# Kernel optimization log

Hardware: AMD Instinct MI355X
Metric: run time of the kernel (lower is better)

## Reference

```python
import jax, jax.numpy as jnp
import numpy as np

N = 20000      # nodes
E = 640000     # edges
IN = 2         # in_dim
H = 4          # heads
C = 64         # hidden_dim (per-head channels)
ED = 3         # edge_dim
K = 4          # num_clusters
EPS = 1e-16    # PyG softmax eps


def setup_inputs():
    key = jax.random.key(0)
    ks = jax.random.split(key, 32)
    g = lambda i, sh: (jax.random.normal(ks[i], sh, dtype=jnp.float32) * 0.1)
    inp = {
        'x': jax.random.normal(ks[0], (N, IN), dtype=jnp.float32),
        'edge_index': jax.random.randint(ks[1], (2, E), 0, N, dtype=jnp.int64),
        'edge_attr': jax.random.normal(ks[2], (E, ED), dtype=jnp.float32),
        # input_proj
        'Wp': g(3, (IN, C)), 'bp': g(4, (C,)),
        # conv1: in C -> H*C, concat
        'W1': g(5, (C, H * C)), 'We1': g(6, (ED, H * C)),
        'as1': g(7, (H, C)), 'ad1': g(8, (H, C)), 'ae1': g(9, (H, C)), 'b1': g(10, (H * C,)),
        # conv2: in H*C -> H*C, concat
        'W2': g(11, (H * C, H * C)), 'We2': g(12, (ED, H * C)),
        'as2': g(13, (H, C)), 'ad2': g(14, (H, C)), 'ae2': g(15, (H, C)), 'b2': g(16, (H * C,)),
        # conv3: in H*C -> C, heads=1
        'W3': g(17, (H * C, C)), 'We3': g(18, (ED, C)),
        'as3': g(19, (1, C)), 'ad3': g(20, (1, C)), 'ae3': g(21, (1, C)), 'b3': g(22, (C,)),
        # classifier
        'Wc': g(23, (C, K)), 'bc': g(24, (K,)),
    }
    return inp


def _gat(h, src, dst, edge_attr, W, We, a_src, a_dst, a_edge, bias, heads, cph):
    """PyG GATConv (shared lin for src/dst, edge_dim, concat=True), eval mode."""
    xh = (h @ W).reshape(N, heads, cph)                       # [N,H,C]
    alpha_src = jnp.einsum('nhc,hc->nh', xh, a_src)           # [N,H]
    alpha_dst = jnp.einsum('nhc,hc->nh', xh, a_dst)
    eh = (edge_attr @ We).reshape(E, heads, cph)              # [E,H,C]
    alpha = alpha_src[src] + alpha_dst[dst] + jnp.einsum('ehc,hc->eh', eh, a_edge)
    alpha = jax.nn.leaky_relu(alpha, 0.2)                     # [E,H]
    # segment softmax over destination neighborhoods
    m = jax.ops.segment_max(alpha, dst, num_segments=N)       # [N,H]
    ea = jnp.exp(alpha - m[dst])
    s = jax.ops.segment_sum(ea, dst, num_segments=N)
    attn = ea / (s[dst] + EPS)                                # [E,H]
    msg = xh[src] * attn[:, :, None]                          # [E,H,C]
    out = jax.ops.segment_sum(msg, dst, num_segments=N)       # [N,H,C]
    return out.reshape(N, heads * cph) + bias


def reference(x, edge_index, edge_attr, Wp, bp,
              W1, We1, as1, ad1, ae1, b1,
              W2, We2, as2, ad2, ae2, b2,
              W3, We3, as3, ad3, ae3, b3,
              Wc, bc):
    src, dst = edge_index[0], edge_index[1]
    h = jax.nn.elu(x @ Wp + bp)
    h = jax.nn.elu(_gat(h, src, dst, edge_attr, W1, We1, as1, ad1, ae1, b1, H, C))
    h = jax.nn.elu(_gat(h, src, dst, edge_attr, W2, We2, as2, ad2, ae2, b2, H, C))
    h = _gat(h, src, dst, edge_attr, W3, We3, as3, ad3, ae3, b3, 1, C)
    return jax.nn.softmax(h @ Wc + bc, axis=-1)
```

## Files before the change

kernel.cpp:

```cpp
#include <hip/hip_runtime.h>
#include <math.h>

#define N_NODES 20000
#define N_EDGES 640000

typedef __attribute__((ext_vector_type(8))) short short8;
typedef __attribute__((ext_vector_type(4))) float floatx4;
typedef __attribute__((ext_vector_type(2))) float float2v;

__device__ __forceinline__ float elu_f(float v) { return v > 0.f ? v : expm1f(v); }

__device__ __forceinline__ unsigned short bf16_rne(float f) {
  union { float f; unsigned u; } v;
  v.f = f;
  unsigned r = v.u + 0x7FFF + ((v.u >> 16) & 1);
  return (unsigned short)(r >> 16);
}

__device__ __forceinline__ float2v unpack_bf2(unsigned u) {
  union { unsigned u; float f; } lo, hi;
  lo.u = u << 16;
  hi.u = u & 0xffff0000u;
  return (float2v){lo.f, hi.f};
}

__device__ __forceinline__ int swz(int c) {
  return (c & ~7) | ((((c & 7) + ((c >> 3) >> 2))) & 7);
}


__global__ void hist_kernel(const int* __restrict__ dst, int* __restrict__ cnt, int ne) {
  int e = blockIdx.x * 256 + threadIdx.x;
  if (e < ne) atomicAdd(&cnt[dst[e]], 1);
}

__global__ __launch_bounds__(1024) void scan_kernel(const int* __restrict__ cnt,
                                                    int* __restrict__ row_ptr,
                                                    int* __restrict__ row_next, int n) {
  __shared__ int part[1024];
  int t = threadIdx.x;
  int per = (n + 1023) / 1024;
  int base = t * per;
  int local = 0;
  for (int i = 0; i < per; ++i) {
    int idx = base + i;
    if (idx < n) local += cnt[idx];
  }
  part[t] = local;
  __syncthreads();
  for (int off = 1; off < 1024; off <<= 1) {
    int v = (t >= off) ? part[t - off] : 0;
    __syncthreads();
    part[t] += v;
    __syncthreads();
  }
  int prefix = (t == 0) ? 0 : part[t - 1];
  for (int i = 0; i < per; ++i) {
    int idx = base + i;
    if (idx < n) {
      row_ptr[idx] = prefix;
      row_next[idx] = prefix;
      prefix += cnt[idx];
    }
  }
  if (t == 1023) row_ptr[n] = part[1023];
}

__global__ void fill_kernel(const int* __restrict__ dst, int* __restrict__ row_next,
                            int* __restrict__ csr_eid, int ne) {
  int e = blockIdx.x * 256 + threadIdx.x;
  if (e >= ne) return;
  int pos = atomicAdd(&row_next[dst[e]], 1);
  csr_eid[pos] = e;
}


__global__ void prep_all_kernel(const float* __restrict__ x, const float* __restrict__ Wp,
                                const float* __restrict__ bp, unsigned short* __restrict__ h_bf,
                                const float* __restrict__ W1, const float* __restrict__ W2,
                                const float* __restrict__ W3, unsigned short* __restrict__ Bt1,
                                unsigned short* __restrict__ Bt2, unsigned short* __restrict__ Bt3,
                                const float* __restrict__ We1, const float* __restrict__ ae1,
                                const float* __restrict__ We2, const float* __restrict__ ae2,
                                const float* __restrict__ We3, const float* __restrict__ ae3,
                                const int* __restrict__ csr_eid, const int* __restrict__ src,
                                const float* __restrict__ ea, int* __restrict__ csr_src,
                                float* __restrict__ edot) {
  int b = blockIdx.x, t = threadIdx.x;
  if (b < 5000) {
    int i = b * 256 + t;
    int node = i >> 6, c = i & 63;
    float v = x[node * 2] * Wp[c] + x[node * 2 + 1] * Wp[64 + c] + bp[c];
    h_bf[i] = bf16_rne(elu_f(v));
  } else if (b < 5384) {
    int idx = (b - 5000) * 256 + t;
    const float* W; unsigned short* Bt; int K, Nc, local;
    if (idx < 16384)      { W = W1; Bt = Bt1; K = 64;  Nc = 256; local = idx; }
    else if (idx < 81920) { W = W2; Bt = Bt2; K = 256; Nc = 256; local = idx - 16384; }
    else if (idx < 98304) { W = W3; Bt = Bt3; K = 256; Nc = 64;  local = idx - 81920; }
    else return;
    int k = local / Nc, n = local - k * Nc;
    Bt[(size_t)n * K + k] = bf16_rne(W[local]);
  } else {
    __shared__ float pj[27];
    if (t < 12) {
      int d = t >> 2, h = t & 3;
      float s = 0.f;
      for (int c = 0; c < 64; ++c) s += We1[d * 256 + h * 64 + c] * ae1[h * 64 + c];
      pj[t] = s;
    } else if (t < 24) {
      int u = t - 12; int d = u >> 2, h = u & 3;
      float s = 0.f;
      for (int c = 0; c < 64; ++c) s += We2[d * 256 + h * 64 + c] * ae2[h * 64 + c];
      pj[12 + u] = s;
    } else if (t < 27) {
      int d = t - 24;
      float s = 0.f;
      for (int c = 0; c < 64; ++c) s += We3[d * 64 + c] * ae3[c];
      pj[24 + d] = s;
    }
    __syncthreads();
    int i = (b - 5384) * 256 + t;
    if (i >= N_EDGES) return;
    int eid = csr_eid[i];
    csr_src[i] = src[eid];
    float e0 = ea[eid * 3 + 0], e1 = ea[eid * 3 + 1], e2 = ea[eid * 3 + 2];
    #pragma unroll
    for (int h = 0; h < 4; ++h)
      edot[(size_t)h * N_EDGES + i] = e0 * pj[h] + e1 * pj[4 + h] + e2 * pj[8 + h];
    #pragma unroll
    for (int h = 0; h < 4; ++h)
      edot[(size_t)(4 + h) * N_EDGES + i] = e0 * pj[12 + h] + e1 * pj[16 + h] + e2 * pj[20 + h];
    edot[(size_t)8 * N_EDGES + i] = e0 * pj[24] + e1 * pj[25] + e2 * pj[26];
  }
}


template <int KDIM>
__global__ __launch_bounds__(256) void mfma_gemm_alpha_kernel(
    const unsigned short* __restrict__ A, const unsigned short* __restrict__ Bt,
    unsigned short* __restrict__ C_bf, const float* __restrict__ a_src,
    const float* __restrict__ a_dst, float* __restrict__ alp_s,
    float* __restrict__ alp_d, int M, int Nc) {
  __shared__ unsigned short As[64][40];
  __shared__ unsigned short Bs[64][40];
  int t = threadIdx.x;
  int wave = t >> 6, lane = t & 63;
  int m_frag = lane & 15, quad = lane >> 4;
  int row0 = blockIdx.y * 64, col0 = blockIdx.x * 64;
  int lr = t >> 2;
  int lk = (t & 3) * 8;
  floatx4 acc[4];
  #pragma unroll
  for (int c = 0; c < 4; ++c) acc[c] = (floatx4){0.f, 0.f, 0.f, 0.f};

  for (int k0 = 0; k0 < KDIM; k0 += 32) {
    int gr = row0 + lr;
    short8 av = {0, 0, 0, 0, 0, 0, 0, 0};
    if (gr < M) av = *(const short8*)(A + (size_t)gr * KDIM + k0 + lk);
    *(short8*)(&As[lr][lk]) = av;
    short8 bv = *(const short8*)(Bt + (size_t)(col0 + lr) * KDIM + k0 + lk);
    *(short8*)(&Bs[lr][lk]) = bv;
    __syncthreads();
    short8 a = *(const short8*)(&As[wave * 16 + m_frag][quad * 8]);
    #pragma unroll
    for (int c = 0; c < 4; ++c) {
      short8 b = *(const short8*)(&Bs[c * 16 + m_frag][quad * 8]);
      acc[c] = __builtin_amdgcn_mfma_f32_16x16x32_bf16(a, b, acc[c], 0, 0, 0);
    }
    __syncthreads();
  }

  int H = Nc >> 6;
  int head = blockIdx.x;
  float ps[4] = {}, pd[4] = {};
  #pragma unroll
  for (int c = 0; c < 4; ++c) {
    float asv = a_src[head * 64 + c * 16 + m_frag];
    float adv = a_dst[head * 64 + c * 16 + m_frag];
    #pragma unroll
    for (int i = 0; i < 4; ++i) {
      ps[i] += acc[c][i] * asv;
      pd[i] += acc[c][i] * adv;
    }
  }
  #pragma unroll
  for (int off = 1; off < 16; off <<= 1) {
    #pragma unroll
    for (int i = 0; i < 4; ++i) {
      ps[i] += __shfl_xor(ps[i], off);
      pd[i] += __shfl_xor(pd[i], off);
    }
  }
  #pragma unroll
  for (int c = 0; c < 4; ++c) {
    #pragma unroll
    for (int i = 0; i < 4; ++i) {
      int gr = row0 + wave * 16 + quad * 4 + i;
      if (gr < M) C_bf[(size_t)gr * Nc + col0 + c * 16 + m_frag] = bf16_rne(acc[c][i]);
    }
  }
  if (m_frag == 0) {
    #pragma unroll
    for (int i = 0; i < 4; ++i) {
      int gr = row0 + wave * 16 + quad * 4 + i;
      if (gr < M) {
        alp_s[gr * H + head] = ps[i];
        alp_d[gr * H + head] = pd[i];
      }
    }
  }
}


template <bool OUT_BF>
__global__ __launch_bounds__(256) void softagg4_kernel(
    const int* __restrict__ row_ptr, const int* __restrict__ csr_src,
    const float* __restrict__ edot, const float* __restrict__ alp_s,
    const float* __restrict__ alp_d, const unsigned short* __restrict__ xh_bf,
    const float* __restrict__ bias, float* __restrict__ out,
    unsigned short* __restrict__ out_bf) {
  constexpr int HC = 256, H = 4, CHUNK = 256, L = 32, S = 8;
  __shared__ float lds_w[H][CHUNK + 8];
  __shared__ int lds_src[CHUNK];
  __shared__ float sh_inv[H];
  __shared__ float red[4 * HC];

  int n = blockIdx.x;
  int t = threadIdx.x;
  int wave = t >> 6, lane = t & 63;
  int slot = t / L, l = t % L;
  int head2 = l >> 3;
  int s0 = row_ptr[n], s1 = row_ptr[n + 1];

  float s_run = 0.f;
  float2v accp[4] = {};
  float adv = alp_d[n * H + wave];
  const float* __restrict__ edot_h = edot + (size_t)wave * N_EDGES;

  for (int c0 = s0; c0 < s1; c0 += CHUNK) {
    int cend = min(s1, c0 + CHUNK);
    {
      float se = 0.f;
      for (int i = c0 + lane; i < cend; i += 64) {
        int s = csr_src[i];
        if (wave == 0) lds_src[i - c0] = s;
        float a = alp_s[s * H + wave] + adv + edot_h[i];
        a = a > 0.f ? a : 0.2f * a;
        float w = __expf(fminf(a, 30.f));
        lds_w[wave][i - c0] = w;
        se += w;
      }
      #pragma unroll
      for (int off = 1; off < 64; off <<= 1) se += __shfl_xor(se, off);
      s_run += se;
    }
    __syncthreads();
    int i = c0 + slot;
    for (; i + S < cend; i += 2 * S) {
      int sA = lds_src[i - c0];
      int sB = lds_src[i - c0 + S];
      float wA = lds_w[head2][i - c0];
      float wB = lds_w[head2][i - c0 + S];
      uint4 uA = *(const uint4*)(xh_bf + (size_t)sA * HC + l * 8);
      uint4 uB = *(const uint4*)(xh_bf + (size_t)sB * HC + l * 8);
      float2v wAp = {wA, wA}, wBp = {wB, wB};
      accp[0] = __builtin_elementwise_fma(unpack_bf2(uA.x), wAp, accp[0]);
      accp[1] = __builtin_elementwise_fma(unpack_bf2(uA.y), wAp, accp[1]);
      accp[2] = __builtin_elementwise_fma(unpack_bf2(uA.z), wAp, accp[2]);
      accp[3] = __builtin_elementwise_fma(unpack_bf2(uA.w), wAp, accp[3]);
      accp[0] = __builtin_elementwise_fma(unpack_bf2(uB.x), wBp, accp[0]);
      accp[1] = __builtin_elementwise_fma(unpack_bf2(uB.y), wBp, accp[1]);
      accp[2] = __builtin_elementwise_fma(unpack_bf2(uB.z), wBp, accp[2]);
      accp[3] = __builtin_elementwise_fma(unpack_bf2(uB.w), wBp, accp[3]);
    }
    if (i < cend) {
      int s = lds_src[i - c0];
      float w = lds_w[head2][i - c0];
      uint4 u = *(const uint4*)(xh_bf + (size_t)s * HC + l * 8);
      float2v wp = {w, w};
      accp[0] = __builtin_elementwise_fma(unpack_bf2(u.x), wp, accp[0]);
      accp[1] = __builtin_elementwise_fma(unpack_bf2(u.y), wp, accp[1]);
      accp[2] = __builtin_elementwise_fma(unpack_bf2(u.z), wp, accp[2]);
      accp[3] = __builtin_elementwise_fma(unpack_bf2(u.w), wp, accp[3]);
    }
    __syncthreads();
  }
  if (lane == 0) sh_inv[wave] = 1.0f / (s_run + 1e-16f);
  __syncthreads();
  float2v invp = {sh_inv[head2], sh_inv[head2]};
  #pragma unroll
  for (int d = 0; d < 4; ++d) accp[d] *= invp;
  float accf[8];
  #pragma unroll
  for (int d = 0; d < 4; ++d) { accf[2 * d] = accp[d].x; accf[2 * d + 1] = accp[d].y; }
  #pragma unroll
  for (int off = L; off < 64; off <<= 1) {
    #pragma unroll
    for (int j = 0; j < 8; ++j) accf[j] += __shfl_xor(accf[j], off);
  }
  if (lane < L) {
    #pragma unroll
    for (int j = 0; j < 8; ++j) red[wave * HC + swz(lane * 8 + j)] = accf[j];
  }
  __syncthreads();
  {
    int pos = swz(t);
    float a = red[0 * HC + pos] + red[1 * HC + pos] + red[2 * HC + pos] + red[3 * HC + pos];
    a += bias[t];
    a = elu_f(a);
    if (OUT_BF) out_bf[(size_t)n * HC + t] = bf16_rne(a);
    else out[(size_t)n * HC + t] = a;
  }
}


__global__ __launch_bounds__(256) void softagg_cls_kernel(
    const int* __restrict__ row_ptr, const int* __restrict__ csr_src,
    const float* __restrict__ edot, const float* __restrict__ alp_s,
    const float* __restrict__ alp_d, const unsigned short* __restrict__ xh_bf,
    const float* __restrict__ b3, const float* __restrict__ Wc,
    const float* __restrict__ bc, float* __restrict__ out, int n_nodes) {
  constexpr int CHUNK = 256;
  __shared__ float lds_w[4][CHUNK];
  __shared__ int lds_s[4][CHUNK];

  int wave = threadIdx.x >> 6, lane = threadIdx.x & 63;
  int n = blockIdx.x * 4 + wave;
  if (n >= n_nodes) return;
  int slot = lane >> 3, l = lane & 7;
  int s0 = row_ptr[n], s1 = row_ptr[n + 1];

  float s_run = 0.f;
  float2v accp[4] = {};
  float adv = alp_d[n];

  for (int c0 = s0; c0 < s1; c0 += CHUNK) {
    int cend = min(s1, c0 + CHUNK);
    float se = 0.f;
    for (int i = c0 + lane; i < cend; i += 64) {
      int s = csr_src[i];
      lds_s[wave][i - c0] = s;
      float a = alp_s[s] + adv + edot[i];
      a = a > 0.f ? a : 0.2f * a;
      float w = __expf(fminf(a, 30.f));
      lds_w[wave][i - c0] = w;
      se += w;
    }
    #pragma unroll
    for (int off = 1; off < 64; off <<= 1) se += __shfl_xor(se, off);
    s_run += se;
    for (int i = c0 + slot; i < cend; i += 8) {
      int s = lds_s[wave][i - c0];
      float w = lds_w[wave][i - c0];
      uint4 u = *(const uint4*)(xh_bf + (size_t)s * 64 + l * 8);
      float2v wp = {w, w};
      accp[0] = __builtin_elementwise_fma(unpack_bf2(u.x), wp, accp[0]);
      accp[1] = __builtin_elementwise_fma(unpack_bf2(u.y), wp, accp[1]);
      accp[2] = __builtin_elementwise_fma(unpack_bf2(u.z), wp, accp[2]);
      accp[3] = __builtin_elementwise_fma(unpack_bf2(u.w), wp, accp[3]);
    }
  }
  float inv = 1.0f / (s_run + 1e-16f);
  float2v invp = {inv, inv};
  #pragma unroll
  for (int d = 0; d < 4; ++d) accp[d] *= invp;
  float accf[8];
  #pragma unroll
  for (int d = 0; d < 4; ++d) { accf[2 * d] = accp[d].x; accf[2 * d + 1] = accp[d].y; }
  #pragma unroll
  for (int off = 8; off < 64; off <<= 1) {
    #pragma unroll
    for (int j = 0; j < 8; ++j) accf[j] += __shfl_xor(accf[j], off);
  }
  float p0 = 0.f, p1 = 0.f, p2 = 0.f, p3 = 0.f;
  #pragma unroll
  for (int j = 0; j < 8; ++j) {
    int c = l * 8 + j;
    float v = accf[j] + b3[c];
    p0 += v * Wc[c * 4 + 0];
    p1 += v * Wc[c * 4 + 1];
    p2 += v * Wc[c * 4 + 2];
    p3 += v * Wc[c * 4 + 3];
  }
  #pragma unroll
  for (int off = 1; off < 8; off <<= 1) {
    p0 += __shfl_xor(p0, off);
    p1 += __shfl_xor(p1, off);
    p2 += __shfl_xor(p2, off);
    p3 += __shfl_xor(p3, off);
  }
  if (lane == 0) {
    p0 += bc[0]; p1 += bc[1]; p2 += bc[2]; p3 += bc[3];
    float mx = fmaxf(fmaxf(p0, p1), fmaxf(p2, p3));
    float e0 = __expf(p0 - mx), e1 = __expf(p1 - mx), e2 = __expf(p2 - mx), e3 = __expf(p3 - mx);
    float s = 1.f / (e0 + e1 + e2 + e3);
    out[n * 4 + 0] = e0 * s;
    out[n * 4 + 1] = e1 * s;
    out[n * 4 + 2] = e2 * s;
    out[n * 4 + 3] = e3 * s;
  }
}


extern "C" void kernel_launch(void* const* d_in, const int* in_sizes, int n_in,
                              void* d_out, int out_size, void* d_ws, size_t ws_size,
                              hipStream_t stream) {
  const float* x   = (const float*)d_in[0];
  const int*   ei  = (const int*)d_in[1];
  const float* ea  = (const float*)d_in[2];
  const float* Wp  = (const float*)d_in[3];
  const float* bp  = (const float*)d_in[4];
  const float* W1  = (const float*)d_in[5];
  const float* We1 = (const float*)d_in[6];
  const float* as1 = (const float*)d_in[7];
  const float* ad1 = (const float*)d_in[8];
  const float* ae1 = (const float*)d_in[9];
  const float* b1  = (const float*)d_in[10];
  const float* W2  = (const float*)d_in[11];
  const float* We2 = (const float*)d_in[12];
  const float* as2 = (const float*)d_in[13];
  const float* ad2 = (const float*)d_in[14];
  const float* ae2 = (const float*)d_in[15];
  const float* b2  = (const float*)d_in[16];
  const float* W3  = (const float*)d_in[17];
  const float* We3 = (const float*)d_in[18];
  const float* as3 = (const float*)d_in[19];
  const float* ad3 = (const float*)d_in[20];
  const float* ae3 = (const float*)d_in[21];
  const float* b3  = (const float*)d_in[22];
  const float* Wc  = (const float*)d_in[23];
  const float* bc  = (const float*)d_in[24];
  float* out = (float*)d_out;

  const int* src = ei;
  const int* dst = ei + N_EDGES;

  char* wptr = (char*)d_ws;
  auto alloc = [&](size_t bytes) {
    char* p = wptr;
    wptr += (bytes + 255) & ~(size_t)255;
    return p;
  };
  int*            cnt      = (int*)alloc((size_t)N_NODES * 4);
  int*            row_ptr  = (int*)alloc((size_t)(N_NODES + 1) * 4);
  int*            row_next = (int*)alloc((size_t)N_NODES * 4);
  int*            csr_eid  = (int*)alloc((size_t)N_EDGES * 4);
  int*            csr_src  = (int*)alloc((size_t)N_EDGES * 4);
  float*          edot     = (float*)alloc((size_t)9 * N_EDGES * 4);
  unsigned short* hA_bf    = (unsigned short*)alloc((size_t)N_NODES * 256 * 2);
  unsigned short* hX_bf    = (unsigned short*)alloc((size_t)N_NODES * 256 * 2);
  float*          alp_s    = (float*)alloc((size_t)N_NODES * 4 * 4);
  float*          alp_d    = (float*)alloc((size_t)N_NODES * 4 * 4);
  unsigned short* Bt1      = (unsigned short*)alloc((size_t)64 * 256 * 2);
  unsigned short* Bt2      = (unsigned short*)alloc((size_t)256 * 256 * 2);
  unsigned short* Bt3      = (unsigned short*)alloc((size_t)256 * 64 * 2);

  hipMemsetAsync(cnt, 0, (size_t)N_NODES * 4, stream);
  hist_kernel<<<(N_EDGES + 255) / 256, 256, 0, stream>>>(dst, cnt, N_EDGES);
  scan_kernel<<<1, 1024, 0, stream>>>(cnt, row_ptr, row_next, N_NODES);
  fill_kernel<<<(N_EDGES + 255) / 256, 256, 0, stream>>>(dst, row_next, csr_eid, N_EDGES);

  prep_all_kernel<<<5384 + (N_EDGES + 255) / 256, 256, 0, stream>>>(
      x, Wp, bp, hA_bf, W1, W2, W3, Bt1, Bt2, Bt3,
      We1, ae1, We2, ae2, We3, ae3, csr_eid, src, ea, csr_src, edot);

  dim3 g256(4, (N_NODES + 63) / 64);
  dim3 g64(1, (N_NODES + 63) / 64);

  mfma_gemm_alpha_kernel<64><<<g256, 256, 0, stream>>>(hA_bf, Bt1, hX_bf, as1, ad1,
                                                       alp_s, alp_d, N_NODES, 256);
  softagg4_kernel<true><<<N_NODES, 256, 0, stream>>>(row_ptr, csr_src,
                                                     edot + (size_t)0 * N_EDGES,
                                                     alp_s, alp_d, hX_bf, b1, nullptr, hA_bf);

  mfma_gemm_alpha_kernel<256><<<g256, 256, 0, stream>>>(hA_bf, Bt2, hX_bf, as2, ad2,
                                                        alp_s, alp_d, N_NODES, 256);
  softagg4_kernel<true><<<N_NODES, 256, 0, stream>>>(row_ptr, csr_src,
                                                     edot + (size_t)4 * N_EDGES,
                                                     alp_s, alp_d, hX_bf, b2, nullptr, hA_bf);

  mfma_gemm_alpha_kernel<256><<<g64, 256, 0, stream>>>(hA_bf, Bt3, hX_bf, as3, ad3,
                                                       alp_s, alp_d, N_NODES, 64);
  softagg_cls_kernel<<<(N_NODES + 3) / 4, 256, 0, stream>>>(row_ptr, csr_src,
                                                            edot + (size_t)8 * N_EDGES,
                                                            alp_s, alp_d, hX_bf, b3, Wc, bc,
                                                            out, N_NODES);
}
```

Baseline: 389.5 us.

## Interleave per-edge head logits and compute all heads per thread in softagg

Stores per-edge attention logit contributions for the 4-head layers as interleaved float4 per edge instead of head-major planes. The softagg score phase now has each thread handle one edge for all four heads, using one csr_src load and float4 loads of alp_s and edot, rather than each wave redundantly reloading csr_src and alp_s for its own head. The per-head normalizer sums are reduced across waves through shared memory with an extra barrier. This cuts redundant gather traffic in the score phase. In exchange it adds a cross-wave reduction, and the LDS weight layout becomes edge-major with a stride of 4.

```diff
diff --git a/kernel.cpp b/kernel.cpp
--- a/kernel.cpp
+++ b/kernel.cpp
@@ -85,7 +85,8 @@
                                 const float* __restrict__ We3, const float* __restrict__ ae3,
                                 const int* __restrict__ csr_eid, const int* __restrict__ src,
                                 const float* __restrict__ ea, int* __restrict__ csr_src,
-                                float* __restrict__ edot) {
+                                float* __restrict__ edot1, float* __restrict__ edot2,
+                                float* __restrict__ edot3) {
   int b = blockIdx.x, t = threadIdx.x;
   if (b < 5000) {
     int i = b * 256 + t;
@@ -125,13 +126,18 @@
     int eid = csr_eid[i];
     csr_src[i] = src[eid];
     float e0 = ea[eid * 3 + 0], e1 = ea[eid * 3 + 1], e2 = ea[eid * 3 + 2];
-    #pragma unroll
-    for (int h = 0; h < 4; ++h)
-      edot[(size_t)h * N_EDGES + i] = e0 * pj[h] + e1 * pj[4 + h] + e2 * pj[8 + h];
-    #pragma unroll
-    for (int h = 0; h < 4; ++h)
-      edot[(size_t)(4 + h) * N_EDGES + i] = e0 * pj[12 + h] + e1 * pj[16 + h] + e2 * pj[20 + h];
-    edot[(size_t)8 * N_EDGES + i] = e0 * pj[24] + e1 * pj[25] + e2 * pj[26];
+    float4 v1, v2;
+    v1.x = e0 * pj[0] + e1 * pj[4] + e2 * pj[8];
+    v1.y = e0 * pj[1] + e1 * pj[5] + e2 * pj[9];
+    v1.z = e0 * pj[2] + e1 * pj[6] + e2 * pj[10];
+    v1.w = e0 * pj[3] + e1 * pj[7] + e2 * pj[11];
+    v2.x = e0 * pj[12] + e1 * pj[16] + e2 * pj[20];
+    v2.y = e0 * pj[13] + e1 * pj[17] + e2 * pj[21];
+    v2.z = e0 * pj[14] + e1 * pj[18] + e2 * pj[22];
+    v2.w = e0 * pj[15] + e1 * pj[19] + e2 * pj[23];
+    *(float4*)(edot1 + (size_t)i * 4) = v1;
+    *(float4*)(edot2 + (size_t)i * 4) = v2;
+    edot3[i] = e0 * pj[24] + e1 * pj[25] + e2 * pj[26];
   }
 }
 
@@ -220,10 +226,11 @@
     const float* __restrict__ alp_d, const unsigned short* __restrict__ xh_bf,
     const float* __restrict__ bias, float* __restrict__ out,
     unsigned short* __restrict__ out_bf) {
-  constexpr int HC = 256, H = 4, CHUNK = 256, L = 32, S = 8;
-  __shared__ float lds_w[H][CHUNK + 8];
+  constexpr int HC = 256, CHUNK = 256, L = 32, S = 8;
+  __shared__ float lds_w[CHUNK * 4];
   __shared__ int lds_src[CHUNK];
-  __shared__ float sh_inv[H];
+  __shared__ float sh_part[4][4];
+  __shared__ float sh_inv[4];
   __shared__ float red[4 * HC];
 
   int n = blockIdx.x;
@@ -233,35 +240,41 @@
   int head2 = l >> 3;
   int s0 = row_ptr[n], s1 = row_ptr[n + 1];
 
-  float s_run = 0.f;
+  float4 adv4 = *(const float4*)(alp_d + n * 4);
+  float s_acc[4] = {};
   float2v accp[4] = {};
-  float adv = alp_d[n * H + wave];
-  const float* __restrict__ edot_h = edot + (size_t)wave * N_EDGES;
 
   for (int c0 = s0; c0 < s1; c0 += CHUNK) {
     int cend = min(s1, c0 + CHUNK);
-    {
-      float se = 0.f;
-      for (int i = c0 + lane; i < cend; i += 64) {
-        int s = csr_src[i];
-        if (wave == 0) lds_src[i - c0] = s;
-        float a = alp_s[s * H + wave] + adv + edot_h[i];
-        a = a > 0.f ? a : 0.2f * a;
-        float w = __expf(fminf(a, 30.f));
-        lds_w[wave][i - c0] = w;
-        se += w;
-      }
-      #pragma unroll
-      for (int off = 1; off < 64; off <<= 1) se += __shfl_xor(se, off);
-      s_run += se;
-    }
-    __syncthreads();
-    int i = c0 + slot;
-    for (; i + S < cend; i += 2 * S) {
-      int sA = lds_src[i - c0];
-      int sB = lds_src[i - c0 + S];
-      float wA = lds_w[head2][i - c0];
-      float wB = lds_w[head2][i - c0 + S];
+    int i = c0 + t;
+    if (i < cend) {
+      int s = csr_src[i];
+      lds_src[t] = s;
+      float4 as4 = *(const float4*)(alp_s + s * 4);
+      float4 ed4 = *(const float4*)(edot + (size_t)i * 4);
+      float a0 = as4.x + adv4.x + ed4.x;
+      float a1 = as4.y + adv4.y + ed4.y;
+      float a2 = as4.z + adv4.z + ed4.z;
+      float a3 = as4.w + adv4.w + ed4.w;
+      a0 = a0 > 0.f ? a0 : 0.2f * a0;
+      a1 = a1 > 0.f ? a1 : 0.2f * a1;
+      a2 = a2 > 0.f ? a2 : 0.2f * a2;
+      a3 = a3 > 0.f ? a3 : 0.2f * a3;
+      float4 w4;
+      w4.x = __expf(fminf(a0, 30.f));
+      w4.y = __expf(fminf(a1, 30.f));
+      w4.z = __expf(fminf(a2, 30.f));
+      w4.w = __expf(fminf(a3, 30.f));
+      *(float4*)(lds_w + t * 4) = w4;
+      s_acc[0] += w4.x; s_acc[1] += w4.y; s_acc[2] += w4.z; s_acc[3] += w4.w;
+    }
+    __syncthreads();
+    int j = c0 + slot;
+    for (; j + S < cend; j += 2 * S) {
+      int sA = lds_src[j - c0];
+      int sB = lds_src[j - c0 + S];
+      float wA = lds_w[(j - c0) * 4 + head2];
+      float wB = lds_w[(j - c0 + S) * 4 + head2];
       uint4 uA = *(const uint4*)(xh_bf + (size_t)sA * HC + l * 8);
       uint4 uB = *(const uint4*)(xh_bf + (size_t)sB * HC + l * 8);
       float2v wAp = {wA, wA}, wBp = {wB, wB};
@@ -274,9 +287,9 @@
       accp[2] = __builtin_elementwise_fma(unpack_bf2(uB.z), wBp, accp[2]);
       accp[3] = __builtin_elementwise_fma(unpack_bf2(uB.w), wBp, accp[3]);
     }
-    if (i < cend) {
-      int s = lds_src[i - c0];
-      float w = lds_w[head2][i - c0];
+    if (j < cend) {
+      int s = lds_src[j - c0];
+      float w = lds_w[(j - c0) * 4 + head2];
       uint4 u = *(const uint4*)(xh_bf + (size_t)s * HC + l * 8);
       float2v wp = {w, w};
       accp[0] = __builtin_elementwise_fma(unpack_bf2(u.x), wp, accp[0]);
@@ -286,7 +299,20 @@
     }
     __syncthreads();
   }
-  if (lane == 0) sh_inv[wave] = 1.0f / (s_run + 1e-16f);
+  #pragma unroll
+  for (int off = 1; off < 64; off <<= 1) {
+    #pragma unroll
+    for (int h = 0; h < 4; ++h) s_acc[h] += __shfl_xor(s_acc[h], off);
+  }
+  if (lane == 0) {
+    #pragma unroll
+    for (int h = 0; h < 4; ++h) sh_part[wave][h] = s_acc[h];
+  }
+  __syncthreads();
+  if (t < 4) {
+    float s = sh_part[0][t] + sh_part[1][t] + sh_part[2][t] + sh_part[3][t];
+    sh_inv[t] = 1.0f / (s + 1e-16f);
+  }
   __syncthreads();
   float2v invp = {sh_inv[head2], sh_inv[head2]};
   #pragma unroll
@@ -447,7 +473,9 @@
   int*            row_next = (int*)alloc((size_t)N_NODES * 4);
   int*            csr_eid  = (int*)alloc((size_t)N_EDGES * 4);
   int*            csr_src  = (int*)alloc((size_t)N_EDGES * 4);
-  float*          edot     = (float*)alloc((size_t)9 * N_EDGES * 4);
+  float*          edot1    = (float*)alloc((size_t)4 * N_EDGES * 4);
+  float*          edot2    = (float*)alloc((size_t)4 * N_EDGES * 4);
+  float*          edot3    = (float*)alloc((size_t)N_EDGES * 4);
   unsigned short* hA_bf    = (unsigned short*)alloc((size_t)N_NODES * 256 * 2);
   unsigned short* hX_bf    = (unsigned short*)alloc((size_t)N_NODES * 256 * 2);
   float*          alp_s    = (float*)alloc((size_t)N_NODES * 4 * 4);
@@ -463,27 +491,24 @@
 
   prep_all_kernel<<<5384 + (N_EDGES + 255) / 256, 256, 0, stream>>>(
       x, Wp, bp, hA_bf, W1, W2, W3, Bt1, Bt2, Bt3,
-      We1, ae1, We2, ae2, We3, ae3, csr_eid, src, ea, csr_src, edot);
+      We1, ae1, We2, ae2, We3, ae3, csr_eid, src, ea, csr_src, edot1, edot2, edot3);
 
   dim3 g256(4, (N_NODES + 63) / 64);
   dim3 g64(1, (N_NODES + 63) / 64);
 
   mfma_gemm_alpha_kernel<64><<<g256, 256, 0, stream>>>(hA_bf, Bt1, hX_bf, as1, ad1,
                                                        alp_s, alp_d, N_NODES, 256);
-  softagg4_kernel<true><<<N_NODES, 256, 0, stream>>>(row_ptr, csr_src,
-                                                     edot + (size_t)0 * N_EDGES,
+  softagg4_kernel<true><<<N_NODES, 256, 0, stream>>>(row_ptr, csr_src, edot1,
                                                      alp_s, alp_d, hX_bf, b1, nullptr, hA_bf);
 
   mfma_gemm_alpha_kernel<256><<<g256, 256, 0, stream>>>(hA_bf, Bt2, hX_bf, as2, ad2,
                                                         alp_s, alp_d, N_NODES, 256);
-  softagg4_kernel<true><<<N_NODES, 256, 0, stream>>>(row_ptr, csr_src,
-                                                     edot + (size_t)4 * N_EDGES,
+  softagg4_kernel<true><<<N_NODES, 256, 0, stream>>>(row_ptr, csr_src, edot2,
                                                      alp_s, alp_d, hX_bf, b2, nullptr, hA_bf);
 
   mfma_gemm_alpha_kernel<256><<<g64, 256, 0, stream>>>(hA_bf, Bt3, hX_bf, as3, ad3,
                                                        alp_s, alp_d, N_NODES, 64);
-  softagg_cls_kernel<<<(N_NODES + 3) / 4, 256, 0, stream>>>(row_ptr, csr_src,
-                                                            edot + (size_t)8 * N_EDGES,
+  softagg_cls_kernel<<<(N_NODES + 3) / 4, 256, 0, stream>>>(row_ptr, csr_src, edot3,
                                                             alp_s, alp_d, hX_bf, b3, Wc, bc,
                                                             out, N_NODES);
 }
```

Measured after the change: 402.1 us. 1.03x slower.
